# Kernel tuning notes

Hardware: AMD Instinct MI355X
Metric: run time of the kernel (lower is better)

The kernel has to match this reference:

```python
import jax, jax.numpy as jnp
import numpy as np

DIM = 1024
HEADS = 16
HD = DIM // HEADS          # 64
SPECIAL = 8                # CLS/register tokens with full attention
GRID = 32                  # 32x32 patch grid
N = SPECIAL + GRID * GRID  # 1032
B = 8
WINDOW = 3                 # 2D sliding-window radius (7x7 box)
EPS = 1e-6


def _make_2d_mask() -> jnp.ndarray:
    """[N, N] bool mask: special tokens attend everywhere; patches use 2D local box."""
    idx = np.arange(N)
    special = (idx[:, None] < SPECIAL) | (idx[None, :] < SPECIAL)
    p = idx - SPECIAL
    r, c = p // GRID, p % GRID
    swa = (np.abs(r[:, None] - r[None, :]) <= WINDOW) & (np.abs(c[:, None] - c[None, :]) <= WINDOW)
    return jnp.asarray(special | swa)

_MASK = _make_2d_mask()


def setup_inputs() -> dict:
    key = jax.random.key(0)
    k1, k2, k3 = jax.random.split(key, 3)
    hidden_states = jax.random.normal(k1, (B, N, DIM), dtype=jnp.float32)
    qkv_w = jax.random.normal(k2, (3 * DIM, DIM), dtype=jnp.float32) * 0.02
    out_w = jax.random.normal(k3, (DIM, DIM), dtype=jnp.float32) * 0.02
    norm_q_w = jnp.ones((HD,), dtype=jnp.float32)
    norm_k_w = jnp.ones((HD,), dtype=jnp.float32)
    # Standard RoPE tables, half-dim frequencies tiled twice (rotate-half convention)
    pos = np.arange(N, dtype=np.float32)
    inv_freq = 1.0 / (10000.0 ** (np.arange(0, HD, 2, dtype=np.float32) / HD))
    ang = pos[:, None] * inv_freq[None, :]              # [N, HD/2]
    freqs_cos = jnp.asarray(np.concatenate([np.cos(ang), np.cos(ang)], axis=-1))  # [N, HD]
    freqs_sin = jnp.asarray(np.concatenate([np.sin(ang), np.sin(ang)], axis=-1))
    return dict(hidden_states=hidden_states, freqs_cos=freqs_cos, freqs_sin=freqs_sin,
                qkv_w=qkv_w, out_w=out_w, norm_q_w=norm_q_w, norm_k_w=norm_k_w)


def _rms_norm(x, w):
    return x * jax.lax.rsqrt(jnp.mean(x * x, axis=-1, keepdims=True) + EPS) * w


def _rotate_half(x):
    return jnp.concatenate([-x[..., HD // 2:], x[..., :HD // 2]], axis=-1)


def reference(hidden_states, freqs_cos, freqs_sin, qkv_w, out_w, norm_q_w, norm_k_w):
    Bn, Nn, C = hidden_states.shape
    # Fused QKV projection -> [3, B, H, N, D]
    qkv = (hidden_states @ qkv_w.T).reshape(Bn, Nn, 3, HEADS, HD).transpose(2, 0, 3, 1, 4)
    q, k, v = qkv[0], qkv[1], qkv[2]
    # per-head-dim RMSNorm on q, k
    q = _rms_norm(q, norm_q_w)
    k = _rms_norm(k, norm_k_w)
    # RoPE
    cos = freqs_cos[None, None]  # [1,1,N,D]
    sin = freqs_sin[None, None]
    q = q * cos + _rotate_half(q) * sin
    k = k * cos + _rotate_half(k) * sin
    # 2D sliding-window + global-token masked attention
    scale = 1.0 / jnp.sqrt(jnp.asarray(HD, dtype=q.dtype))
    scores = jnp.einsum('bhqd,bhkd->bhqk', q, k) * scale
    neg = jnp.asarray(jnp.finfo(scores.dtype).min, scores.dtype)
    scores = jnp.where(_MASK[None, None], scores, neg)
    probs = jax.nn.softmax(scores, axis=-1)
    attn = jnp.einsum('bhqk,bhkd->bhqd', probs, v)
    attn = attn.transpose(0, 2, 1, 3).reshape(Bn, Nn, C)
    return attn @ out_w.T
```

## Files before the change

kernel.cpp:

```cpp
#include <hip/hip_runtime.h>
#include <hip/hip_bf16.h>

typedef unsigned short ushort_t;
typedef __bf16 bf16x8 __attribute__((ext_vector_type(8)));
typedef float f32x4 __attribute__((ext_vector_type(4)));
typedef float f32x8 __attribute__((ext_vector_type(8)));

#define NTOK 1032
#define NROWS 8256
#define DIMC 1024
#define QKV_ELEMS 8454144
#define XE 8454144
#define QWE 3145728
#define OWE 1048576

__device__ __forceinline__ float bf2f(ushort_t u) {
    union { unsigned int i; float f; } v; v.i = ((unsigned int)u) << 16; return v.f;
}
__device__ __forceinline__ ushort_t f2bf(float f) {
    union { float f; unsigned int i; } v; v.f = f;
    unsigned int r = v.i + 0x7fffu + ((v.i >> 16) & 1u);
    return (ushort_t)(r >> 16);
}
__device__ __forceinline__ bf16x8 cvt8(const float* p) {
    const float4 a = *(const float4*)p;
    const float4 b = *(const float4*)(p + 4);
    bf16x8 r;
    r[0] = (__bf16)a.x; r[1] = (__bf16)a.y; r[2] = (__bf16)a.z; r[3] = (__bf16)a.w;
    r[4] = (__bf16)b.x; r[5] = (__bf16)b.y; r[6] = (__bf16)b.z; r[7] = (__bf16)b.w;
    return r;
}
__device__ __forceinline__ void load_lds16(const ushort_t* g, ushort_t* l) {
    __builtin_amdgcn_global_load_lds(
        (const __attribute__((address_space(1))) unsigned int*)g,
        (__attribute__((address_space(3))) unsigned int*)l, 16, 0, 0);
}

__global__ __launch_bounds__(256) void cvt_kernel(
    const float* __restrict__ X, const float* __restrict__ Wq,
    const float* __restrict__ Wo,
    ushort_t* __restrict__ Xb, ushort_t* __restrict__ Wqb,
    ushort_t* __restrict__ Wob)
{
    const long i8 = ((long)blockIdx.x * 256 + threadIdx.x) * 8;
    const float* src;
    ushort_t* dst;
    long off;
    if (i8 < XE)            { src = X;  dst = Xb;  off = i8; }
    else if (i8 < XE + QWE) { src = Wq; dst = Wqb; off = i8 - XE; }
    else                    { src = Wo; dst = Wob; off = i8 - XE - QWE; }
    *(bf16x8*)(dst + off) = cvt8(src + off);
}

template<int MODE>
__device__ __forceinline__ void gemm256_body(
    const ushort_t* __restrict__ A, const ushort_t* __restrict__ W,
    ushort_t* __restrict__ QKV, float* __restrict__ Out,
    const float* __restrict__ cosb, const float* __restrict__ sinb,
    const float* __restrict__ nqw, const float* __restrict__ nkw)
{
    constexpr int SMEM_BYTES = (MODE == 0) ? 135168 : 131072;
    __shared__ __align__(16) unsigned char SMEM[SMEM_BYTES];
    ushort_t* A_lds = (ushort_t*)SMEM;
    ushort_t* B_lds = (ushort_t*)(SMEM + 65536);

    constexpr int GX  = (MODE == 0) ? 12 : 4;
    constexpr int NWG = GX * 33;
    constexpr int QW  = NWG >> 3, RW = NWG & 7;
    const int orig = blockIdx.y * GX + blockIdx.x;
    const int xcd  = orig & 7, li = orig >> 3;
    const int wgid = (xcd < RW ? xcd * (QW + 1)
                               : RW * (QW + 1) + (xcd - RW) * QW) + li;
    const int bx = wgid % GX, by = wgid / GX;

    const int tid  = threadIdx.x;
    const int wave = tid >> 6, lane = tid & 63;
    const int wr = wave >> 2, wc = wave & 3;
    const int fr = lane & 15, quad = lane >> 4;
    const int m0 = by * 256;
    const int n0 = bx * 256;
    const bool swap = (MODE == 1) || (bx < 8);

    int aoff[4], boff[4];
    #pragma unroll
    for (int ld = 0; ld < 4; ++ld) {
        const int s   = ld * 512 + tid;
        const int row = s >> 3;
        const int kc  = ((s & 7) ^ (row & 7)) * 8;
        int ar = m0 + row; if (ar > NROWS - 1) ar = NROWS - 1;
        aoff[ld] = ar * DIMC + kc;
        boff[ld] = (n0 + row) * DIMC + kc;
    }

    const int ck0 = (quad ^ (fr & 7)) * 8;
    const int ck1 = ((quad + 4) ^ (fr & 7)) * 8;
    const int abase = (wr * 128 + fr) * 64;
    const int bbase = (wc * 64 + fr) * 64;

    f32x4 acc[8][4] = {};

#define SA(ld, t, c) load_lds16(A + aoff[ld] + (t) * 64, \
                                &A_lds[(c) * 16384 + ((ld) * 512 + tid) * 8])
#define SB(ld, t, c) load_lds16(W + boff[ld] + (t) * 64, \
                                &B_lds[(c) * 16384 + ((ld) * 512 + tid) * 8])
#define WAIT_LGKM0 asm volatile("s_waitcnt lgkmcnt(0)" ::: "memory")
#define WAIT_VM6   asm volatile("s_waitcnt vmcnt(6)"  ::: "memory")
#define WAIT_VM0   asm volatile("s_waitcnt vmcnt(0)"  ::: "memory")

#define READ_AF(p) \
    af[0][0] = *(const bf16x8*)&A_lds[cb + abase + ((p) * 2 + 0) * 1024 + ck0]; \
    af[0][1] = *(const bf16x8*)&A_lds[cb + abase + ((p) * 2 + 0) * 1024 + ck1]; \
    af[1][0] = *(const bf16x8*)&A_lds[cb + abase + ((p) * 2 + 1) * 1024 + ck0]; \
    af[1][1] = *(const bf16x8*)&A_lds[cb + abase + ((p) * 2 + 1) * 1024 + ck1];

#define MFMA_PHASE(p) \
    __builtin_amdgcn_s_setprio(1); \
    if (swap) { \
        _Pragma("unroll") \
        for (int mfi = 0; mfi < 2; ++mfi) \
            _Pragma("unroll") \
            for (int nf = 0; nf < 4; ++nf) { \
                acc[(p) * 2 + mfi][nf] = __builtin_amdgcn_mfma_f32_16x16x32_bf16( \
                    bfrag[nf][0], af[mfi][0], acc[(p) * 2 + mfi][nf], 0, 0, 0); \
                acc[(p) * 2 + mfi][nf] = __builtin_amdgcn_mfma_f32_16x16x32_bf16( \
                    bfrag[nf][1], af[mfi][1], acc[(p) * 2 + mfi][nf], 0, 0, 0); \
            } \
    } else { \
        _Pragma("unroll") \
        for (int mfi = 0; mfi < 2; ++mfi) \
            _Pragma("unroll") \
            for (int nf = 0; nf < 4; ++nf) { \
                acc[(p) * 2 + mfi][nf] = __builtin_amdgcn_mfma_f32_16x16x32_bf16( \
                    af[mfi][0], bfrag[nf][0], acc[(p) * 2 + mfi][nf], 0, 0, 0); \
                acc[(p) * 2 + mfi][nf] = __builtin_amdgcn_mfma_f32_16x16x32_bf16( \
                    af[mfi][1], bfrag[nf][1], acc[(p) * 2 + mfi][nf], 0, 0, 0); \
            } \
    } \
    __builtin_amdgcn_s_setprio(0);

    SB(0, 0, 0); SB(1, 0, 0); SB(2, 0, 0); SB(3, 0, 0);
    SA(0, 0, 0); SA(1, 0, 0); SA(2, 0, 0); SA(3, 0, 0);
    SB(0, 1, 1); SB(1, 1, 1); SB(2, 1, 1); SB(3, 1, 1);
    SA(0, 1, 1); SA(2, 1, 1);
    WAIT_VM6;
    __builtin_amdgcn_s_barrier();

    for (int t = 0; t < 16; ++t) {
        const int c = t & 1, o = c ^ 1;
        const int cb = c * 16384;
        bf16x8 bfrag[4][2];
        bf16x8 af[2][2];

        #pragma unroll
        for (int nf = 0; nf < 4; ++nf) {
            bfrag[nf][0] = *(const bf16x8*)&B_lds[cb + bbase + nf * 1024 + ck0];
            bfrag[nf][1] = *(const bf16x8*)&B_lds[cb + bbase + nf * 1024 + ck1];
        }
        READ_AF(0);
        if (t < 15) { SA(1, t + 1, o); SA(3, t + 1, o); }
        __builtin_amdgcn_s_barrier();
        WAIT_LGKM0; __builtin_amdgcn_sched_barrier(0);
        MFMA_PHASE(0);
        __builtin_amdgcn_s_barrier();

        READ_AF(1);
        if (t < 14) { SB(0, t + 2, c); SB(1, t + 2, c);
                      SB(2, t + 2, c); SB(3, t + 2, c); }
        __builtin_amdgcn_s_barrier();
        WAIT_LGKM0; __builtin_amdgcn_sched_barrier(0);
        MFMA_PHASE(1);
        __builtin_amdgcn_s_barrier();

        READ_AF(2);
        if (t < 14) { SA(0, t + 2, c); SA(2, t + 2, c); }
        __builtin_amdgcn_s_barrier();
        WAIT_LGKM0; __builtin_amdgcn_sched_barrier(0);
        MFMA_PHASE(2);

        READ_AF(3);
        __builtin_amdgcn_s_barrier();
        WAIT_LGKM0; __builtin_amdgcn_sched_barrier(0);
        MFMA_PHASE(3);

        if (t < 14)       { WAIT_VM6; __builtin_amdgcn_s_barrier(); }
        else if (t == 14) { WAIT_VM0; __builtin_amdgcn_s_barrier(); }
    }

    const int rb = quad * 4;
    if (MODE == 1) {
        #pragma unroll
        for (int mf = 0; mf < 8; ++mf) {
            const int m = m0 + wr * 128 + mf * 16 + fr;
            if (m < NROWS) {
                #pragma unroll
                for (int nf = 0; nf < 4; ++nf) {
                    const int o_ = n0 + wc * 64 + nf * 16 + rb;
                    float4 pk;
                    pk.x = acc[mf][nf][0];
                    pk.y = acc[mf][nf][1];
                    pk.z = acc[mf][nf][2];
                    pk.w = acc[mf][nf][3];
                    *(float4*)(Out + (long)m * DIMC + o_) = pk;
                }
            }
        }
    } else if (swap) {
        const int part   = n0 >> 10;
        const int hgbase = ((n0 & 1023) + wc * 64) >> 6;
        const float* wtab = (part == 0) ? nqw : nkw;

        float* T = (float*)SMEM;
        __syncthreads();
        for (int e = tid; e < 256 * 16; e += 512) {
            const int row = e >> 4, seg = e & 15;
            const int mm  = m0 + row;
            const int bb2 = mm / NTOK;
            const int n2  = mm - bb2 * NTOK;
            const float4 c4 = *(const float4*)(cosb + n2 * 64 + seg * 4);
            const float4 s4 = *(const float4*)(sinb + n2 * 64 + seg * 4);
            const float4 wf = *(const float4*)(wtab + seg * 4);
            const float4 wp = *(const float4*)(wtab + ((seg ^ 8) * 4));
            float* dst = T + row * 132 + seg * 8;
            ((float2*)dst)[0] = make_float2(c4.x * wf.x, s4.x * wp.x);
            ((float2*)dst)[1] = make_float2(c4.y * wf.y, s4.y * wp.y);
            ((float2*)dst)[2] = make_float2(c4.z * wf.z, s4.z * wp.z);
            ((float2*)dst)[3] = make_float2(c4.w * wf.w, s4.w * wp.w);
        }
        __syncthreads();

#define QK_NF(MF, NF, PN, SGN) { \
        const float4 q0 = *(const float4*)(trow + ((NF) * 16 + rb) * 2); \
        const float4 q1 = *(const float4*)(trow + ((NF) * 16 + rb) * 2 + 4); \
        ushort4 pk; \
        pk.x = f2bf(rms * (acc[MF][NF][0] * q0.x + (SGN) * acc[MF][PN][0] * q0.y)); \
        pk.y = f2bf(rms * (acc[MF][NF][1] * q0.z + (SGN) * acc[MF][PN][1] * q0.w)); \
        pk.z = f2bf(rms * (acc[MF][NF][2] * q1.x + (SGN) * acc[MF][PN][2] * q1.y)); \
        pk.w = f2bf(rms * (acc[MF][NF][3] * q1.z + (SGN) * acc[MF][PN][3] * q1.w)); \
        *(ushort4*)(outb + (NF) * 16) = pk; }

#define QK_MF(MF) { \
        const int rr = wr * 128 + (MF) * 16 + fr; \
        const int m  = m0 + rr; \
        if (m < NROWS) { \
            const int bb = m / NTOK, n = m - bb * NTOK; \
            float ss = 0.f; \
            _Pragma("unroll") \
            for (int nf = 0; nf < 4; ++nf) { \
                ss += acc[MF][nf][0] * acc[MF][nf][0]; \
                ss += acc[MF][nf][1] * acc[MF][nf][1]; \
                ss += acc[MF][nf][2] * acc[MF][nf][2]; \
                ss += acc[MF][nf][3] * acc[MF][nf][3]; \
            } \
            ss += __shfl_xor(ss, 16, 64); \
            ss += __shfl_xor(ss, 32, 64); \
            const float rms = rsqrtf(ss * (1.0f / 64.0f) + 1e-6f); \
            const float* trow = T + rr * 132; \
            ushort_t* outb = QKV + (long)part * QKV_ELEMS + \
                ((long)(bb * 16 + hgbase) * NTOK + n) * 64 + rb; \
            QK_NF(MF, 0, 2, -1.f) \
            QK_NF(MF, 1, 3, -1.f) \
            QK_NF(MF, 2, 0,  1.f) \
            QK_NF(MF, 3, 1,  1.f) \
        } }

        QK_MF(0) QK_MF(1) QK_MF(2) QK_MF(3)
        QK_MF(4) QK_MF(5) QK_MF(6) QK_MF(7)
#undef QK_MF
#undef QK_NF
    } else {
        const int hg = ((n0 & 1023) + wc * 64) >> 6;
        #pragma unroll
        for (int nf = 0; nf < 4; ++nf) {
            const int d = nf * 16 + fr;
            #pragma unroll
            for (int mf = 0; mf < 8; ++mf) {
                const int mb = m0 + wr * 128 + mf * 16 + rb;
                if (mb < NROWS) {
                    const int bb = mb / NTOK, n = mb - bb * NTOK;
                    ushort4 pk;
                    pk.x = f2bf(acc[mf][nf][0]);
                    pk.y = f2bf(acc[mf][nf][1]);
                    pk.z = f2bf(acc[mf][nf][2]);
                    pk.w = f2bf(acc[mf][nf][3]);
                    *(ushort4*)(QKV + 2L * QKV_ELEMS +
                        ((long)((bb * 16 + hg) * 64 + d)) * NTOK + n) = pk;
                }
            }
        }
    }
#undef SA
#undef SB
#undef WAIT_LGKM0
#undef WAIT_VM6
#undef WAIT_VM0
#undef READ_AF
#undef MFMA_PHASE
}

__global__ __launch_bounds__(512, 2) void gemm_qkv_kernel(
    const ushort_t* __restrict__ A, const ushort_t* __restrict__ W,
    ushort_t* __restrict__ QKV,
    const float* __restrict__ cosb, const float* __restrict__ sinb,
    const float* __restrict__ nqw, const float* __restrict__ nkw)
{
    gemm256_body<0>(A, W, QKV, nullptr, cosb, sinb, nqw, nkw);
}

__global__ __launch_bounds__(512, 2) void gemm_out_kernel(
    const ushort_t* __restrict__ A, const ushort_t* __restrict__ W,
    float* __restrict__ Out)
{
    gemm256_body<1>(A, W, nullptr, Out, nullptr, nullptr, nullptr, nullptr);
}

__global__ __launch_bounds__(256) void attn_kernel(
    const ushort_t* __restrict__ Qb, const ushort_t* __restrict__ Kb,
    const ushort_t* __restrict__ Vt, ushort_t* __restrict__ AO)
{
    __shared__ __align__(16) ushort_t Ks[232 * 68];
    __shared__ __align__(16) ushort_t Vs[64 * 236];
    __shared__ __align__(16) ushort_t Ps[32 * 280];

    const int tid = threadIdx.x;
    const int wave = tid >> 6, lane = tid & 63;
    const int m_ = lane & 15, quad = lane >> 4;
    const int nb = wave * 64;
    const int d0 = wave * 16;

    bf16x8 ones;
    #pragma unroll
    for (int e = 0; e < 8; ++e) ones[e] = (__bf16)1.0f;

    if (blockIdx.x >= 128) {
        const int blk = blockIdx.x - 128;
        const int bh = blk & 127, qr = blk >> 7;
        const int b = bh >> 4, h = bh & 15;

        int r0 = qr - 3; if (r0 < 0) r0 = 0;
        int r1 = qr + 3; if (r1 > 31) r1 = 31;
        const int limit = 8 + (r1 - r0 + 1) * 32;
        const int nch = limit >> 3;

        const ushort_t* Qg  = Qb + ((long)bh * NTOK + 8 + qr * 32) * 64;
        const ushort_t* Kg  = Kb + (long)bh * NTOK * 64;
        const ushort_t* Vtg = Vt + (long)bh * 64 * NTOK;

        bf16x8 af[2][2];
        #pragma unroll
        for (int mt = 0; mt < 2; ++mt)
            #pragma unroll
            for (int ks = 0; ks < 2; ++ks)
                af[mt][ks] = *(const bf16x8*)(Qg + (mt * 16 + m_) * 64 + ks * 32 + quad * 8);

        for (int c = tid; c < limit * 8; c += 256) {
            const int slot = c >> 3, c8 = (c & 7) * 8;
            const int tok = slot + (slot >= 8 ? r0 * 32 : 0);
            *(bf16x8*)&Ks[slot * 68 + c8] = *(const bf16x8*)(Kg + (long)tok * 64 + c8);
        }
        for (int e = tid; e < 64 * 32; e += 256) {
            const int d = e >> 5, j = e & 31;
            if (j < nch) {
                const int tok = (j == 0) ? 0 : 8 + r0 * 32 + (j - 1) * 8;
                *(bf16x8*)&Vs[d * 236 + j * 8] =
                    *(const bf16x8*)(Vtg + (long)d * NTOK + tok);
            }
        }
        __syncthreads();

        bf16x8 bfr[4][2];
        #pragma unroll
        for (int nt = 0; nt < 4; ++nt) {
            const int slot = nb + nt * 16 + m_;
            const int srow = (slot < limit) ? slot : 0;
            #pragma unroll
            for (int ks = 0; ks < 2; ++ks)
                bfr[nt][ks] = *(const bf16x8*)&Ks[srow * 68 + ks * 32 + quad * 8];
        }

        f32x4 sacc[2][4] = {};
        #pragma unroll
        for (int mt = 0; mt < 2; ++mt)
            #pragma unroll
            for (int nt = 0; nt < 4; ++nt) {
                sacc[mt][nt] = __builtin_amdgcn_mfma_f32_16x16x32_bf16(
                    af[mt][0], bfr[nt][0], sacc[mt][nt], 0, 0, 0);
                sacc[mt][nt] = __builtin_amdgcn_mfma_f32_16x16x32_bf16(
                    af[mt][1], bfr[nt][1], sacc[mt][nt], 0, 0, 0);
            }

        #pragma unroll
        for (int mt = 0; mt < 2; ++mt)
            #pragma unroll
            for (int nt = 0; nt < 4; ++nt) {
                const int slot = nb + nt * 16 + m_;
                const int kc = (slot - 8) & 31;
                #pragma unroll
                for (int reg = 0; reg < 4; ++reg) {
                    const int qm = mt * 16 + quad * 4 + reg;
                    const bool val = (slot < 8) ||
                        ((slot < limit) && ((unsigned)(kc - qm + 3) <= 6u));
                    const float p = val ? __expf(sacc[mt][nt][reg] * 0.125f) : 0.f;
                    Ps[qm * 280 + slot] = f2bf(p);
                }
            }
        __syncthreads();

        f32x4 oacc[2] = {}, lacc[2] = {};
        #pragma unroll
        for (int ks = 0; ks < 8; ++ks) {
            const int slot0 = ks * 32 + quad * 8;
            const int col0 = (slot0 < limit) ? slot0 : 0;
            const bf16x8 bv = *(const bf16x8*)&Vs[(d0 + m_) * 236 + col0];
            #pragma unroll
            for (int mt = 0; mt < 2; ++mt) {
                const bf16x8 ap = *(const bf16x8*)&Ps[(mt * 16 + m_) * 280 + ks * 32 + quad * 8];
                oacc[mt] = __builtin_amdgcn_mfma_f32_16x16x32_bf16(ap, bv, oacc[mt], 0, 0, 0);
                lacc[mt] = __builtin_amdgcn_mfma_f32_16x16x32_bf16(ap, ones, lacc[mt], 0, 0, 0);
            }
        }
        #pragma unroll
        for (int mt = 0; mt < 2; ++mt)
            #pragma unroll
            for (int reg = 0; reg < 4; ++reg) {
                const int qm = mt * 16 + quad * 4 + reg;
                const int tok = 8 + qr * 32 + qm;
                AO[((long)(b * NTOK + tok)) * DIMC + h * 64 + d0 + m_] =
                    f2bf(oacc[mt][reg] / lacc[mt][reg]);
            }
    } else {
        const int bh = blockIdx.x;
        const int b = bh >> 4, h = bh & 15;
        const ushort_t* Kg  = Kb + (long)bh * NTOK * 64;
        const ushort_t* Vtg = Vt + (long)bh * 64 * NTOK;

        bf16x8 afs[2];
        if (m_ < 8) {
            #pragma unroll
            for (int ks = 0; ks < 2; ++ks)
                afs[ks] = *(const bf16x8*)(Qb + ((long)bh * NTOK + m_) * 64 + ks * 32 + quad * 8);
        } else {
            #pragma unroll
            for (int ks = 0; ks < 2; ++ks)
                #pragma unroll
                for (int e = 0; e < 8; ++e) afs[ks][e] = (__bf16)0.f;
        }

        f32x4 oacc = {}, lacc = {};
        for (int ch = 0; ch < 5; ++ch) {
            const int tok0 = ch * 256;
            const int limit = (NTOK - tok0 < 256) ? (NTOK - tok0) : 256;

            bf16x8 bfr[4][2];
            #pragma unroll
            for (int nt = 0; nt < 4; ++nt) {
                const int slot = nb + nt * 16 + m_;
                const int tok = tok0 + ((slot < limit) ? slot : 0);
                #pragma unroll
                for (int ks = 0; ks < 2; ++ks)
                    bfr[nt][ks] = *(const bf16x8*)(Kg + (long)tok * 64 + ks * 32 + quad * 8);
            }
            f32x4 sacc[4] = {};
            #pragma unroll
            for (int nt = 0; nt < 4; ++nt) {
                sacc[nt] = __builtin_amdgcn_mfma_f32_16x16x32_bf16(afs[0], bfr[nt][0], sacc[nt], 0, 0, 0);
                sacc[nt] = __builtin_amdgcn_mfma_f32_16x16x32_bf16(afs[1], bfr[nt][1], sacc[nt], 0, 0, 0);
            }

            bf16x8 bv[8];
            #pragma unroll
            for (int ks = 0; ks < 8; ++ks) {
                const int slot0 = ks * 32 + quad * 8;
                const int tok = tok0 + ((slot0 < limit) ? slot0 : 0);
                bv[ks] = *(const bf16x8*)(Vtg + (long)(d0 + m_) * NTOK + tok);
            }

            __syncthreads();
            #pragma unroll
            for (int nt = 0; nt < 4; ++nt) {
                const int slot = nb + nt * 16 + m_;
                const bool val = (slot < limit);
                #pragma unroll
                for (int reg = 0; reg < 4; ++reg) {
                    const int qm = quad * 4 + reg;
                    const float p = val ? __expf(sacc[nt][reg] * 0.125f) : 0.f;
                    Ps[qm * 280 + slot] = f2bf(p);
                }
            }
            __syncthreads();

            #pragma unroll
            for (int ks = 0; ks < 8; ++ks) {
                const bf16x8 ap = *(const bf16x8*)&Ps[m_ * 280 + ks * 32 + quad * 8];
                oacc = __builtin_amdgcn_mfma_f32_16x16x32_bf16(ap, bv[ks], oacc, 0, 0, 0);
                lacc = __builtin_amdgcn_mfma_f32_16x16x32_bf16(ap, ones,   lacc, 0, 0, 0);
            }
        }

        #pragma unroll
        for (int reg = 0; reg < 4; ++reg) {
            const int qm = quad * 4 + reg;
            if (qm < 8) {
                AO[((long)(b * NTOK + qm)) * DIMC + h * 64 + d0 + m_] =
                    f2bf(oacc[reg] / lacc[reg]);
            }
        }
    }
}

extern "C" void kernel_launch(void* const* d_in, const int* in_sizes, int n_in,
                              void* d_out, int out_size, void* d_ws, size_t ws_size,
                              hipStream_t stream) {
    const float* X    = (const float*)d_in[0];
    const float* fc   = (const float*)d_in[1];
    const float* fs   = (const float*)d_in[2];
    const float* qkvw = (const float*)d_in[3];
    const float* outw = (const float*)d_in[4];
    const float* nqw  = (const float*)d_in[5];
    const float* nkw  = (const float*)d_in[6];

    ushort_t* Qb  = (ushort_t*)d_ws;
    ushort_t* Kb  = Qb + QKV_ELEMS;
    ushort_t* Vt  = Kb + QKV_ELEMS;
    ushort_t* AO  = Vt + QKV_ELEMS;
    ushort_t* Xb  = AO + QKV_ELEMS;
    ushort_t* Wqb = Xb + XE;
    ushort_t* Wob = Wqb + QWE;
    float* Out = (float*)d_out;

    cvt_kernel<<<6176, 256, 0, stream>>>(X, qkvw, outw, Xb, Wqb, Wob);
    gemm_qkv_kernel<<<dim3(12, 33), 512, 0, stream>>>(Xb, Wqb, Qb, fc, fs, nqw, nkw);
    attn_kernel<<<4224, 256, 0, stream>>>(Qb, Kb, Vt, AO);
    gemm_out_kernel<<<dim3(4, 33), 512, 0, stream>>>(AO, Wob, Out);
}
```

Measured before the change: 273.7 us.

## Assign one query-row tile per wave in attention, drop shared K/V staging

The windowed attention path now gives each wave a whole (batch, head, query-row) tile instead of splitting one tile across four waves. K and V fragments are read straight from global memory into registers rather than staged through shared memory, and each wave keeps its own private P buffer. This removes the block-wide __syncthreads and the LDS copies, and the grid shrinks from 4224 to 1152 blocks. In exchange, each wave does four times the MFMA work serially, and K/V reads go through global/L2 with less coalescing. The special-token path keeps the old scheme with a narrower P stride.

```diff
diff --git a/kernel.cpp b/kernel.cpp
--- a/kernel.cpp
+++ b/kernel.cpp
@@ -317,33 +317,29 @@
     const ushort_t* __restrict__ Qb, const ushort_t* __restrict__ Kb,
     const ushort_t* __restrict__ Vt, ushort_t* __restrict__ AO)
 {
-    __shared__ __align__(16) ushort_t Ks[232 * 68];
-    __shared__ __align__(16) ushort_t Vs[64 * 236];
-    __shared__ __align__(16) ushort_t Ps[32 * 280];
+    __shared__ __align__(16) ushort_t Ps[4 * 32 * 264];
 
     const int tid = threadIdx.x;
     const int wave = tid >> 6, lane = tid & 63;
     const int m_ = lane & 15, quad = lane >> 4;
-    const int nb = wave * 64;
-    const int d0 = wave * 16;
 
     bf16x8 ones;
     #pragma unroll
     for (int e = 0; e < 8; ++e) ones[e] = (__bf16)1.0f;
 
     if (blockIdx.x >= 128) {
-        const int blk = blockIdx.x - 128;
-        const int bh = blk & 127, qr = blk >> 7;
+        const int t4 = (blockIdx.x - 128) * 4 + wave;
+        const int bh = t4 & 127, qr = t4 >> 7;
         const int b = bh >> 4, h = bh & 15;
 
         int r0 = qr - 3; if (r0 < 0) r0 = 0;
         int r1 = qr + 3; if (r1 > 31) r1 = 31;
         const int limit = 8 + (r1 - r0 + 1) * 32;
-        const int nch = limit >> 3;
 
         const ushort_t* Qg  = Qb + ((long)bh * NTOK + 8 + qr * 32) * 64;
         const ushort_t* Kg  = Kb + (long)bh * NTOK * 64;
         const ushort_t* Vtg = Vt + (long)bh * 64 * NTOK;
+        ushort_t* Pw = Ps + wave * (32 * 264);
 
         bf16x8 af[2][2];
         #pragma unroll
@@ -352,82 +348,81 @@
             for (int ks = 0; ks < 2; ++ks)
                 af[mt][ks] = *(const bf16x8*)(Qg + (mt * 16 + m_) * 64 + ks * 32 + quad * 8);
 
-        for (int c = tid; c < limit * 8; c += 256) {
-            const int slot = c >> 3, c8 = (c & 7) * 8;
-            const int tok = slot + (slot >= 8 ? r0 * 32 : 0);
-            *(bf16x8*)&Ks[slot * 68 + c8] = *(const bf16x8*)(Kg + (long)tok * 64 + c8);
-        }
-        for (int e = tid; e < 64 * 32; e += 256) {
-            const int d = e >> 5, j = e & 31;
-            if (j < nch) {
-                const int tok = (j == 0) ? 0 : 8 + r0 * 32 + (j - 1) * 8;
-                *(bf16x8*)&Vs[d * 236 + j * 8] =
-                    *(const bf16x8*)(Vtg + (long)d * NTOK + tok);
-            }
-        }
-        __syncthreads();
-
-        bf16x8 bfr[4][2];
-        #pragma unroll
-        for (int nt = 0; nt < 4; ++nt) {
-            const int slot = nb + nt * 16 + m_;
-            const int srow = (slot < limit) ? slot : 0;
-            #pragma unroll
-            for (int ks = 0; ks < 2; ++ks)
-                bfr[nt][ks] = *(const bf16x8*)&Ks[srow * 68 + ks * 32 + quad * 8];
-        }
-
-        f32x4 sacc[2][4] = {};
-        #pragma unroll
-        for (int mt = 0; mt < 2; ++mt)
-            #pragma unroll
-            for (int nt = 0; nt < 4; ++nt) {
-                sacc[mt][nt] = __builtin_amdgcn_mfma_f32_16x16x32_bf16(
-                    af[mt][0], bfr[nt][0], sacc[mt][nt], 0, 0, 0);
-                sacc[mt][nt] = __builtin_amdgcn_mfma_f32_16x16x32_bf16(
-                    af[mt][1], bfr[nt][1], sacc[mt][nt], 0, 0, 0);
-            }
-
-        #pragma unroll
-        for (int mt = 0; mt < 2; ++mt)
-            #pragma unroll
-            for (int nt = 0; nt < 4; ++nt) {
-                const int slot = nb + nt * 16 + m_;
+        #pragma unroll
+        for (int nt = 0; nt < 16; ++nt) {
+            const int slot = nt * 16 + m_;
+            if (nt * 16 < limit) {
+                int tok = (slot < 8) ? slot : (slot + r0 * 32);
+                if (slot >= limit) tok = 0;
+                const bf16x8 b0 = *(const bf16x8*)(Kg + (long)tok * 64 + quad * 8);
+                const bf16x8 b1 = *(const bf16x8*)(Kg + (long)tok * 64 + 32 + quad * 8);
+                f32x4 s0 = {}, s1 = {};
+                s0 = __builtin_amdgcn_mfma_f32_16x16x32_bf16(af[0][0], b0, s0, 0, 0, 0);
+                s0 = __builtin_amdgcn_mfma_f32_16x16x32_bf16(af[0][1], b1, s0, 0, 0, 0);
+                s1 = __builtin_amdgcn_mfma_f32_16x16x32_bf16(af[1][0], b0, s1, 0, 0, 0);
+                s1 = __builtin_amdgcn_mfma_f32_16x16x32_bf16(af[1][1], b1, s1, 0, 0, 0);
                 const int kc = (slot - 8) & 31;
                 #pragma unroll
                 for (int reg = 0; reg < 4; ++reg) {
-                    const int qm = mt * 16 + quad * 4 + reg;
-                    const bool val = (slot < 8) ||
-                        ((slot < limit) && ((unsigned)(kc - qm + 3) <= 6u));
-                    const float p = val ? __expf(sacc[mt][nt][reg] * 0.125f) : 0.f;
-                    Ps[qm * 280 + slot] = f2bf(p);
+                    const int qm0 = quad * 4 + reg;
+                    const bool v0 = (slot < 8) ||
+                        ((slot < limit) && ((unsigned)(kc - qm0 + 3) <= 6u));
+                    Pw[qm0 * 264 + slot] = f2bf(v0 ? __expf(s0[reg] * 0.125f) : 0.f);
+                    const int qm1 = 16 + qm0;
+                    const bool v1 = (slot < 8) ||
+                        ((slot < limit) && ((unsigned)(kc - qm1 + 3) <= 6u));
+                    Pw[qm1 * 264 + slot] = f2bf(v1 ? __expf(s1[reg] * 0.125f) : 0.f);
                 }
-            }
-        __syncthreads();
-
-        f32x4 oacc[2] = {}, lacc[2] = {};
+            } else {
+                #pragma unroll
+                for (int reg = 0; reg < 4; ++reg) {
+                    const int qm0 = quad * 4 + reg;
+                    Pw[qm0 * 264 + slot] = 0;
+                    Pw[(16 + qm0) * 264 + slot] = 0;
+                }
+            }
+        }
+
+        asm volatile("s_waitcnt lgkmcnt(0)" ::: "memory");
+        __builtin_amdgcn_sched_barrier(0);
+
+        f32x4 oacc[2][4] = {};
+        f32x4 lacc[2] = {};
         #pragma unroll
         for (int ks = 0; ks < 8; ++ks) {
             const int slot0 = ks * 32 + quad * 8;
-            const int col0 = (slot0 < limit) ? slot0 : 0;
-            const bf16x8 bv = *(const bf16x8*)&Vs[(d0 + m_) * 236 + col0];
-            #pragma unroll
-            for (int mt = 0; mt < 2; ++mt) {
-                const bf16x8 ap = *(const bf16x8*)&Ps[(mt * 16 + m_) * 280 + ks * 32 + quad * 8];
-                oacc[mt] = __builtin_amdgcn_mfma_f32_16x16x32_bf16(ap, bv, oacc[mt], 0, 0, 0);
-                lacc[mt] = __builtin_amdgcn_mfma_f32_16x16x32_bf16(ap, ones, lacc[mt], 0, 0, 0);
-            }
-        }
+            int tokv;
+            if (slot0 >= limit) tokv = 0;
+            else if (slot0 < 8) tokv = slot0;
+            else tokv = 8 + r0 * 32 + (slot0 - 8);
+            const bf16x8 ap0 = *(const bf16x8*)&Pw[(m_) * 264 + slot0];
+            const bf16x8 ap1 = *(const bf16x8*)&Pw[(16 + m_) * 264 + slot0];
+            #pragma unroll
+            for (int db = 0; db < 4; ++db) {
+                const bf16x8 bv = *(const bf16x8*)(Vtg + (long)(db * 16 + m_) * NTOK + tokv);
+                oacc[0][db] = __builtin_amdgcn_mfma_f32_16x16x32_bf16(ap0, bv, oacc[0][db], 0, 0, 0);
+                oacc[1][db] = __builtin_amdgcn_mfma_f32_16x16x32_bf16(ap1, bv, oacc[1][db], 0, 0, 0);
+            }
+            lacc[0] = __builtin_amdgcn_mfma_f32_16x16x32_bf16(ap0, ones, lacc[0], 0, 0, 0);
+            lacc[1] = __builtin_amdgcn_mfma_f32_16x16x32_bf16(ap1, ones, lacc[1], 0, 0, 0);
+        }
+
         #pragma unroll
         for (int mt = 0; mt < 2; ++mt)
             #pragma unroll
             for (int reg = 0; reg < 4; ++reg) {
                 const int qm = mt * 16 + quad * 4 + reg;
                 const int tok = 8 + qr * 32 + qm;
-                AO[((long)(b * NTOK + tok)) * DIMC + h * 64 + d0 + m_] =
-                    f2bf(oacc[mt][reg] / lacc[mt][reg]);
+                const float inv = 1.0f / lacc[mt][reg];
+                #pragma unroll
+                for (int db = 0; db < 4; ++db) {
+                    AO[((long)(b * NTOK + tok)) * DIMC + h * 64 + db * 16 + m_] =
+                        f2bf(oacc[mt][db][reg] * inv);
+                }
             }
     } else {
+        const int nb = wave * 64;
+        const int d0 = wave * 16;
         const int bh = blockIdx.x;
         const int b = bh >> 4, h = bh & 15;
         const ushort_t* Kg  = Kb + (long)bh * NTOK * 64;
@@ -483,14 +478,14 @@
                 for (int reg = 0; reg < 4; ++reg) {
                     const int qm = quad * 4 + reg;
                     const float p = val ? __expf(sacc[nt][reg] * 0.125f) : 0.f;
-                    Ps[qm * 280 + slot] = f2bf(p);
+                    Ps[qm * 264 + slot] = f2bf(p);
                 }
             }
             __syncthreads();
 
             #pragma unroll
             for (int ks = 0; ks < 8; ++ks) {
-                const bf16x8 ap = *(const bf16x8*)&Ps[m_ * 280 + ks * 32 + quad * 8];
+                const bf16x8 ap = *(const bf16x8*)&Ps[m_ * 264 + ks * 32 + quad * 8];
                 oacc = __builtin_amdgcn_mfma_f32_16x16x32_bf16(ap, bv[ks], oacc, 0, 0, 0);
                 lacc = __builtin_amdgcn_mfma_f32_16x16x32_bf16(ap, ones,   lacc, 0, 0, 0);
             }
@@ -529,6 +524,6 @@
 
     cvt_kernel<<<6176, 256, 0, stream>>>(X, qkvw, outw, Xb, Wqb, Wob);
     gemm_qkv_kernel<<<dim3(12, 33), 512, 0, stream>>>(Xb, Wqb, Qb, fc, fs, nqw, nkw);
-    attn_kernel<<<4224, 256, 0, stream>>>(Qb, Kb, Vt, AO);
+    attn_kernel<<<1152, 256, 0, stream>>>(Qb, Kb, Vt, AO);
     gemm_out_kernel<<<dim3(4, 33), 512, 0, stream>>>(AO, Wob, Out);
 }
```

Measured after the change: 250.6 us. -8.4%, faster.
